# Optimization experiments

Hardware: AMD Instinct MI355X
Metric: run time of the kernel (lower is better)

Reference implementation:

```python
import jax, jax.numpy as jnp
import numpy as np

B, S, D, H, L, I, V, T = 8, 512, 768, 12, 6, 3072, 30522, 2
DH = D // H  # 64


def ln2d(x, g, b, eps=1e-5):
    # LayerNorm over the last two dims ([S, D]), affine params shaped [S, D]
    mu = jnp.mean(x, axis=(-2, -1), keepdims=True)
    var = jnp.var(x, axis=(-2, -1), keepdims=True)
    return (x - mu) * jax.lax.rsqrt(var + eps) * g + b


def setup_inputs() -> dict:
    key = jax.random.key(0)
    ks = jax.random.split(key, 16)
    s = 0.02
    inp = {
        "input_ids": jax.random.randint(ks[0], (B, S), 0, V, dtype=jnp.int32),
        "segment_ids": jax.random.randint(ks[1], (B, S), 0, T, dtype=jnp.int32),
        "input_mask": jnp.ones((B, S), dtype=jnp.float32),
        "word_emb": jax.random.normal(ks[2], (V, D), jnp.float32) * s,
        "seg_emb": jax.random.normal(ks[3], (T, D), jnp.float32) * s,
        "pos_emb": jax.random.normal(ks[4], (S, D), jnp.float32) * s,
        "ln0_g": jnp.ones((S, D), jnp.float32),
        "ln0_b": jnp.zeros((S, D), jnp.float32),
        "Wq": jax.random.normal(ks[5], (L, D, D), jnp.float32) * s,
        "Wk": jax.random.normal(ks[6], (L, D, D), jnp.float32) * s,
        "Wv": jax.random.normal(ks[7], (L, D, D), jnp.float32) * s,
        "W1": jax.random.normal(ks[8], (L, D, D), jnp.float32) * s,
        "b1": jnp.zeros((L, D), jnp.float32),
        "Wi": jax.random.normal(ks[9], (L, D, I), jnp.float32) * s,
        "bi": jnp.zeros((L, I), jnp.float32),
        "W2": jax.random.normal(ks[10], (L, I, D), jnp.float32) * s,
        "b2": jnp.zeros((L, D), jnp.float32),
        "lng": jnp.ones((L, S, D), jnp.float32),
        "lnb": jnp.zeros((L, S, D), jnp.float32),
        "Wp": jax.random.normal(ks[11], (D, 2), jnp.float32) * s,
        "bp": jnp.zeros((2,), jnp.float32),
    }
    return inp


def _forward(input_ids, segment_ids, input_mask, word_emb, seg_emb, pos_emb,
             ln0_g, ln0_b, Wq, Wk, Wv, W1, b1, Wi, bi, W2, b2, lng, lnb, Wp, bp):
    # embedding (word + segment + position), then 2-D LayerNorm
    x = word_emb[input_ids] + seg_emb[segment_ids] + pos_emb  # [B,S,D]
    x = ln2d(x, ln0_g, ln0_b)
    # multiplicative attention mask, broadcast over heads and KEY axis
    qmask = input_mask[:, None, :, None]  # [B,1,S,1]
    scale = 1.0 / jnp.sqrt(jnp.asarray(DH, x.dtype))
    for l in range(L):
        prev = x
        q = (x @ Wq[l]).reshape(B, S, H, DH).transpose(0, 2, 1, 3)
        k = (x @ Wk[l]).reshape(B, S, H, DH).transpose(0, 2, 1, 3)
        v = (x @ Wv[l]).reshape(B, S, H, DH).transpose(0, 2, 1, 3)
        scores = jnp.einsum('bhqd,bhkd->bhqk', q, k) * scale
        scores = scores * qmask  # multiplicative mask (as in source)
        probs = jax.nn.softmax(scores, axis=-1)
        attn = jnp.einsum('bhqk,bhkd->bhqd', probs, v)
        attn = attn.transpose(0, 2, 1, 3).reshape(B, S, D)
        h = jax.nn.relu(attn @ W1[l] + b1[l])
        h = jax.nn.relu(h @ Wi[l] + bi[l])
        h = jax.nn.relu(h @ W2[l] + b2[l])
        x = ln2d(h + prev, lng[l], lnb[l])
    logits = x @ Wp + bp  # [B,S,2]
    logits = logits + (1.0 - input_mask)[:, :, None] * (-1e4)
    return logits[:, :, 0], logits[:, :, 1]


def reference(input_ids, segment_ids, input_mask, word_emb, seg_emb, pos_emb,
              ln0_g, ln0_b, Wq, Wk, Wv, W1, b1, Wi, bi, W2, b2, lng, lnb, Wp, bp):
    return _forward(input_ids, segment_ids, input_mask, word_emb, seg_emb, pos_emb,
                    ln0_g, ln0_b, Wq, Wk, Wv, W1, b1, Wi, bi, W2, b2, lng, lnb, Wp, bp)
```

## Files before the change

### kernel.cpp

```cpp
#include <hip/hip_runtime.h>
#include <cstdint>
#include <cstddef>

typedef __bf16 bf16x8 __attribute__((ext_vector_type(8)));
typedef float f32x4 __attribute__((ext_vector_type(4)));
typedef unsigned short u16;

#define NB 8
#define NS 512
#define ND 768
#define NH 12
#define NL 6
#define NI 3072
#define NROWS (NB*NS)
#define SD (NS*ND)
#define MN ((size_t)NROWS*ND)

__device__ __forceinline__ u16 f2bf(float f) {
  union { float f; unsigned u; } v; v.f = f;
  unsigned r = v.u + 0x7fffu + ((v.u >> 16) & 1u);
  return (u16)(r >> 16);
}
__device__ __forceinline__ float b2f(u16 u) {
  union { unsigned u; float f; } v; v.u = ((unsigned)u) << 16; return v.f;
}

#define GLL(gsrc, ldst) \
  __builtin_amdgcn_global_load_lds((__attribute__((address_space(1))) void*)(gsrc), \
                                   (__attribute__((address_space(3))) void*)(ldst), 16, 0, 0)

#define CHS 4168

__global__ __launch_bounds__(256) void wconv_k(
    const float* __restrict__ Wq, const float* __restrict__ Wk, const float* __restrict__ Wv,
    const float* __restrict__ W1, const float* __restrict__ Wi, const float* __restrict__ W2,
    u16* __restrict__ wqkv_t, u16* __restrict__ w1_t, u16* __restrict__ wi_t, u16* __restrict__ w2_t)
{
  int bid = blockIdx.x;
  int l = bid / 864, r = bid % 864;
  const float* src; u16* dst; int Csrc, dstLD, tr, tc;
  if (r < 216) {
    int which = r / 72, t2 = r % 72;
    src = (which == 0 ? Wq : (which == 1 ? Wk : Wv)) + (size_t)l * ND * ND;
    dst = wqkv_t + (size_t)l * 2304 * ND + (size_t)which * ND * ND;
    Csrc = ND; dstLD = ND; tr = t2 / 12; tc = t2 % 12;
  } else if (r < 288) {
    int t2 = r - 216;
    src = W1 + (size_t)l * ND * ND; dst = w1_t + (size_t)l * ND * ND;
    Csrc = ND; dstLD = ND; tr = t2 / 12; tc = t2 % 12;
  } else if (r < 576) {
    int t2 = r - 288;
    src = Wi + (size_t)l * ND * NI; dst = wi_t + (size_t)l * ND * NI;
    Csrc = NI; dstLD = ND; tr = t2 / 48; tc = t2 % 48;
  } else {
    int t2 = r - 576;
    src = W2 + (size_t)l * ND * NI; dst = w2_t + (size_t)l * ND * NI;
    Csrc = ND; dstLD = NI; tr = t2 / 12; tc = t2 % 12;
  }
  __shared__ u16 lds[2 * CHS];
  int t0 = threadIdx.x;
  {
    int rrow = t0 >> 3, c0 = (t0 & 7) * 8;
    float4 va[4], vb[4];
    #pragma unroll
    for (int q = 0; q < 4; q++) {
      const float* sp = src + (size_t)(tr * 128 + q * 32 + rrow) * Csrc + tc * 64 + c0;
      va[q] = *reinterpret_cast<const float4*>(sp);
      vb[q] = *reinterpret_cast<const float4*>(sp + 4);
    }
    #pragma unroll
    for (int q = 0; q < 4; q++) {
      int row = q * 32 + rrow;
      u16* lp = &lds[(row >> 6) * CHS + (row & 63) * 65 + c0];
      lp[0] = f2bf(va[q].x); lp[1] = f2bf(va[q].y); lp[2] = f2bf(va[q].z); lp[3] = f2bf(va[q].w);
      lp[4] = f2bf(vb[q].x); lp[5] = f2bf(vb[q].y); lp[6] = f2bf(vb[q].z); lp[7] = f2bf(vb[q].w);
    }
  }
  __syncthreads();
  {
    int qq = t0 & 15;
    int rb = t0 >> 4;
    int ch = qq >> 3;
    int r6b = (qq & 7) * 8;
    #pragma unroll
    for (int p = 0; p < 4; p++) {
      int dstrow = p * 16 + rb;
      const u16* lq = &lds[ch * CHS + dstrow];
      unsigned res[4];
      #pragma unroll
      for (int e = 0; e < 4; e++) {
        unsigned lo = lq[(r6b + 2 * e) * 65];
        unsigned hi = lq[(r6b + 2 * e + 1) * 65];
        res[e] = lo | (hi << 16);
      }
      u16* dp = dst + (size_t)(tc * 64 + dstrow) * dstLD + tr * 128 + qq * 8;
      *reinterpret_cast<uint4*>(dp) = make_uint4(res[0], res[1], res[2], res[3]);
    }
  }
}

__global__ __launch_bounds__(256) void embed_ln_k(const int* __restrict__ ids,
    const int* __restrict__ segs, const float* __restrict__ wemb,
    const float* __restrict__ semb, const float* __restrict__ pemb,
    float* __restrict__ out, float* __restrict__ part)
{
  int b = blockIdx.x >> 6, c = blockIdx.x & 63;
  int base_row = b * NS + c * 8;
  int t = threadIdx.x;
  float s = 0.f, sq = 0.f;
  #pragma unroll
  for (int j = 0; j < 6; j++) {
    int fi = t + j * 256;
    int riw = fi / 192, col4 = fi - riw * 192;
    int row = base_row + riw;
    int id = ids[row], sg = segs[row];
    int srow = row & (NS - 1);
    float4 a = reinterpret_cast<const float4*>(wemb + (size_t)id * ND)[col4];
    float4 bb = reinterpret_cast<const float4*>(semb + (size_t)sg * ND)[col4];
    float4 cc = reinterpret_cast<const float4*>(pemb + (size_t)srow * ND)[col4];
    float y0 = a.x + bb.x + cc.x, y1 = a.y + bb.y + cc.y;
    float y2 = a.z + bb.z + cc.z, y3 = a.w + bb.w + cc.w;
    float4 o; o.x = y0; o.y = y1; o.z = y2; o.w = y3;
    reinterpret_cast<float4*>(out)[(size_t)row * 192 + col4] = o;
    s += y0 + y1 + y2 + y3;
    sq += y0 * y0 + y1 * y1 + y2 * y2 + y3 * y3;
  }
  #pragma unroll
  for (int d = 1; d < 64; d <<= 1) { s += __shfl_xor(s, d); sq += __shfl_xor(sq, d); }
  __shared__ float red[8];
  int w = t >> 6, lane = t & 63;
  if (lane == 0) { red[w] = s; red[4 + w] = sq; }
  __syncthreads();
  if (t == 0) {
    part[blockIdx.x * 2 + 0] = red[0] + red[1] + red[2] + red[3];
    part[blockIdx.x * 2 + 1] = red[4] + red[5] + red[6] + red[7];
  }
}

__global__ __launch_bounds__(256) void ln_apply_k(const float* __restrict__ x,
    const float* __restrict__ g, const float* __restrict__ bta, const float* __restrict__ part,
    u16* __restrict__ xb)
{
  int idx = blockIdx.x * 256 + threadIdx.x;
  int e = idx * 4;
  int b = e / SD;
  int sd = e - b * SD;
  int lane = threadIdx.x & 63;
  float s = part[b * 128 + lane * 2 + 0];
  float q = part[b * 128 + lane * 2 + 1];
  #pragma unroll
  for (int d = 1; d < 64; d <<= 1) { s += __shfl_xor(s, d); q += __shfl_xor(q, d); }
  float inv = 1.f / (float)SD;
  float mu = s * inv;
  float rstd = rsqrtf(q * inv - mu * mu + 1e-5f);
  float4 v = reinterpret_cast<const float4*>(x)[idx];
  float4 gg = reinterpret_cast<const float4*>(g)[sd >> 2];
  float4 bb = reinterpret_cast<const float4*>(bta)[sd >> 2];
  float y0 = (v.x - mu) * rstd * gg.x + bb.x;
  float y1 = (v.y - mu) * rstd * gg.y + bb.y;
  float y2 = (v.z - mu) * rstd * gg.z + bb.z;
  float y3 = (v.w - mu) * rstd * gg.w + bb.w;
  reinterpret_cast<ushort4*>(xb)[idx] = make_ushort4(f2bf(y0), f2bf(y1), f2bf(y2), f2bf(y3));
}

__global__ __launch_bounds__(256) void finw1_k(const u16* __restrict__ P,
    const float* __restrict__ bias, u16* __restrict__ out)
{
  size_t idx = (size_t)blockIdx.x * 256 + threadIdx.x;
  ushort4 p0 = reinterpret_cast<const ushort4*>(P)[idx];
  ushort4 p1 = reinterpret_cast<const ushort4*>(P)[idx + (MN >> 2)];
  ushort4 p2 = reinterpret_cast<const ushort4*>(P)[idx + 2 * (MN >> 2)];
  ushort4 p3 = reinterpret_cast<const ushort4*>(P)[idx + 3 * (MN >> 2)];
  int col4 = (int)((idx * 4) % ND) >> 2;
  float4 bv = reinterpret_cast<const float4*>(bias)[col4];
  float y0 = fmaxf(b2f(p0.x) + b2f(p1.x) + b2f(p2.x) + b2f(p3.x) + bv.x, 0.f);
  float y1 = fmaxf(b2f(p0.y) + b2f(p1.y) + b2f(p2.y) + b2f(p3.y) + bv.y, 0.f);
  float y2 = fmaxf(b2f(p0.z) + b2f(p1.z) + b2f(p2.z) + b2f(p3.z) + bv.z, 0.f);
  float y3 = fmaxf(b2f(p0.w) + b2f(p1.w) + b2f(p2.w) + b2f(p3.w) + bv.w, 0.f);
  reinterpret_cast<ushort4*>(out)[idx] = make_ushort4(f2bf(y0), f2bf(y1), f2bf(y2), f2bf(y3));
}

__global__ __launch_bounds__(256) void finw2_k(const u16* __restrict__ P,
    const float* __restrict__ bias, const u16* __restrict__ resid,
    float* __restrict__ ln_in, float* __restrict__ part)
{
  int b = blockIdx.x >> 6, c = blockIdx.x & 63;
  size_t f4base = ((size_t)b * SD + (size_t)c * 6144) >> 2;
  int t = threadIdx.x;
  float s = 0.f, sq = 0.f;
  #pragma unroll
  for (int j = 0; j < 6; j++) {
    size_t fi = f4base + t + j * 256;
    ushort4 p0 = reinterpret_cast<const ushort4*>(P)[fi];
    ushort4 p1 = reinterpret_cast<const ushort4*>(P)[fi + (MN >> 2)];
    ushort4 p2 = reinterpret_cast<const ushort4*>(P)[fi + 2 * (MN >> 2)];
    ushort4 p3 = reinterpret_cast<const ushort4*>(P)[fi + 3 * (MN >> 2)];
    ushort4 rv = reinterpret_cast<const ushort4*>(resid)[fi];
    int col4 = (((t + j * 256) * 4) % ND) >> 2;
    float4 bv = reinterpret_cast<const float4*>(bias)[col4];
    float y0 = fmaxf(b2f(p0.x) + b2f(p1.x) + b2f(p2.x) + b2f(p3.x) + bv.x, 0.f) + b2f(rv.x);
    float y1 = fmaxf(b2f(p0.y) + b2f(p1.y) + b2f(p2.y) + b2f(p3.y) + bv.y, 0.f) + b2f(rv.y);
    float y2 = fmaxf(b2f(p0.z) + b2f(p1.z) + b2f(p2.z) + b2f(p3.z) + bv.z, 0.f) + b2f(rv.z);
    float y3 = fmaxf(b2f(p0.w) + b2f(p1.w) + b2f(p2.w) + b2f(p3.w) + bv.w, 0.f) + b2f(rv.w);
    float4 o; o.x = y0; o.y = y1; o.z = y2; o.w = y3;
    reinterpret_cast<float4*>(ln_in)[fi] = o;
    s += y0 + y1 + y2 + y3;
    sq += y0 * y0 + y1 * y1 + y2 * y2 + y3 * y3;
  }
  #pragma unroll
  for (int d = 1; d < 64; d <<= 1) { s += __shfl_xor(s, d); sq += __shfl_xor(sq, d); }
  __shared__ float red[8];
  int w = t >> 6, lane = t & 63;
  if (lane == 0) { red[w] = s; red[4 + w] = sq; }
  __syncthreads();
  if (t == 0) {
    part[blockIdx.x * 2 + 0] = red[0] + red[1] + red[2] + red[3];
    part[blockIdx.x * 2 + 1] = red[4] + red[5] + red[6] + red[7];
  }
}

#define BM 128
#define BN 128
#define BK 32

template<int EPI>
__global__ __launch_bounds__(256) void gemm_bt(
    const u16* __restrict__ A, const u16* __restrict__ Bt, void* __restrict__ Cv,
    const float* __restrict__ bias, int M, int N, int K)
{
  __shared__ __align__(16) u16 As[2][BM * BK];
  __shared__ __align__(16) u16 Bs[2][BN * BK];
  const int gx = gridDim.x, gy = gridDim.y;
  int wg = (blockIdx.z * gy + blockIdx.y) * gx + blockIdx.x;
  int nwg = gx * gy * gridDim.z;
  int L = (wg & 7) * (nwg >> 3) + (wg >> 3);
  const int bx = L % gx, by = (L / gx) % gy, bz = L / (gx * gy);

  const int t = threadIdx.x;
  const int lane = t & 63, w = t >> 6;
  const int wr = w >> 1, wc = w & 1;
  const int l15 = lane & 15, lh = lane >> 4;
  const int m0 = by * BM, n0 = bx * BN;
  const int Ksub = K / gridDim.z;
  const int Koff = bz * Ksub;

  f32x4 acc[4][4];
  const f32x4 z4 = {0.f, 0.f, 0.f, 0.f};
  #pragma unroll
  for (int i = 0; i < 4; i++)
    #pragma unroll
    for (int j = 0; j < 4; j++) acc[i][j] = z4;

  const int ca = t, cb = t + 256;
  const u16* a0p = A + (size_t)(m0 + (ca >> 2)) * K + (ca & 3) * 8 + Koff;
  const u16* a1p = A + (size_t)(m0 + (cb >> 2)) * K + (cb & 3) * 8 + Koff;
  const u16* b0p = Bt + (size_t)(n0 + (ca >> 2)) * K + (ca & 3) * 8 + Koff;
  const u16* b1p = Bt + (size_t)(n0 + (cb >> 2)) * K + (cb & 3) * 8 + Koff;

  auto stage = [&](int buf, int k0) {
    GLL(a0p + k0, &As[buf][ca * 8]);
    GLL(a1p + k0, &As[buf][cb * 8]);
    GLL(b0p + k0, &Bs[buf][ca * 8]);
    GLL(b1p + k0, &Bs[buf][cb * 8]);
  };

  const int nt = Ksub / BK;
  stage(0, 0);
  __syncthreads();
  for (int it = 0; it < nt; ++it) {
    const int cur = it & 1;
    if (it + 1 < nt) stage(cur ^ 1, (it + 1) * BK);
    bf16x8 af[4], bfr[4];
    #pragma unroll
    for (int i = 0; i < 4; i++)
      af[i] = *reinterpret_cast<const bf16x8*>(&As[cur][(wr * 64 + i * 16 + l15) * BK + lh * 8]);
    #pragma unroll
    for (int j = 0; j < 4; j++)
      bfr[j] = *reinterpret_cast<const bf16x8*>(&Bs[cur][(wc * 64 + j * 16 + l15) * BK + lh * 8]);
    #pragma unroll
    for (int i = 0; i < 4; i++)
      #pragma unroll
      for (int j = 0; j < 4; j++)
        acc[i][j] = __builtin_amdgcn_mfma_f32_16x16x32_bf16(af[i], bfr[j], acc[i][j], 0, 0, 0);
    __syncthreads();
  }

  u16* PoutB = (u16*)Cv + (size_t)bz * M * N;
  #pragma unroll
  for (int i = 0; i < 4; i++) {
    int row_b = m0 + wr * 64 + i * 16 + lh * 4;
    #pragma unroll
    for (int j = 0; j < 4; j++) {
      int col = n0 + wc * 64 + j * 16 + l15;
      float bv = (EPI == 1) ? bias[col] : 0.f;
      #pragma unroll
      for (int r = 0; r < 4; r++) {
        size_t off = (size_t)(row_b + r) * N + col;
        float v = acc[i][j][r];
        if (EPI == 1) ((u16*)Cv)[off] = f2bf(fmaxf(v + bv, 0.f));
        else if (EPI == 3) PoutB[off] = f2bf(v);
        else ((u16*)Cv)[off] = f2bf(v);
      }
    }
  }
}

__global__ __launch_bounds__(256) void attn_k(
    const u16* __restrict__ qkv, const float* __restrict__ mask, u16* __restrict__ out)
{
  int wg = (blockIdx.z * 12 + blockIdx.y) * 8 + blockIdx.x;
  int L = (wg & 7) * 96 + (wg >> 3);
  const int qt = L & 7;
  const int h = (L >> 3) % 12;
  const int b = L / 96;
  __shared__ __align__(16) u16 Qs[64 * 64];
  __shared__ __align__(16) u16 Ks[64 * 72];
  __shared__ __align__(16) u16 Vt[64 * 72];
  __shared__ __align__(16) u16 Pw[4][16 * 72];
  const int t = threadIdx.x, lane = t & 63, w = t >> 6;
  const int l15 = lane & 15, lh = lane >> 4;

  #pragma unroll
  for (int p = 0; p < 2; p++) {
    int c = t + p * 256;
    const u16* src = qkv + (size_t)(b * NS + qt * 64 + (c >> 3)) * 2304 + h * 64 + (c & 7) * 8;
    GLL(src, Qs + c * 8);
  }
  __syncthreads();

  bf16x8 aq[2];
  #pragma unroll
  for (int kk = 0; kk < 2; kk++)
    aq[kk] = *reinterpret_cast<const bf16x8*>(&Qs[(w * 16 + l15) * 64 + kk * 32 + lh * 8]);

  float qm[4];
  #pragma unroll
  for (int r = 0; r < 4; r++)
    qm[r] = mask[b * NS + qt * 64 + w * 16 + lh * 4 + r] * 0.125f;

  float mrun[4], lrun[4];
  f32x4 o[4];
  const f32x4 z4 = {0.f, 0.f, 0.f, 0.f};
  #pragma unroll
  for (int r = 0; r < 4; r++) { mrun[r] = -3e38f; lrun[r] = 0.f; }
  #pragma unroll
  for (int jn = 0; jn < 4; jn++) o[jn] = z4;

  for (int kc = 0; kc < 8; kc++) {
    __syncthreads();
    #pragma unroll
    for (int p = 0; p < 2; p++) {
      int k = (t >> 3) + p * 32;
      int dh0 = (t & 7) * 8;
      const u16* ks = qkv + (size_t)(b * NS + kc * 64 + k) * 2304 + ND + h * 64 + dh0;
      uint4 kv4 = *reinterpret_cast<const uint4*>(ks);
      *reinterpret_cast<uint4*>(&Ks[k * 72 + dh0]) = kv4;
    }
    #pragma unroll
    for (int p = 0; p < 2; p++) {
      int k = (t >> 3) + p * 32;
      int dh0 = (t & 7) * 8;
      const u16* vs = qkv + (size_t)(b * NS + kc * 64 + k) * 2304 + 2 * ND + h * 64 + dh0;
      uint4 vv = *reinterpret_cast<const uint4*>(vs);
      Vt[(dh0 + 0) * 72 + k] = (u16)(vv.x & 0xffff);
      Vt[(dh0 + 1) * 72 + k] = (u16)(vv.x >> 16);
      Vt[(dh0 + 2) * 72 + k] = (u16)(vv.y & 0xffff);
      Vt[(dh0 + 3) * 72 + k] = (u16)(vv.y >> 16);
      Vt[(dh0 + 4) * 72 + k] = (u16)(vv.z & 0xffff);
      Vt[(dh0 + 5) * 72 + k] = (u16)(vv.z >> 16);
      Vt[(dh0 + 6) * 72 + k] = (u16)(vv.w & 0xffff);
      Vt[(dh0 + 7) * 72 + k] = (u16)(vv.w >> 16);
    }
    __syncthreads();

    f32x4 s[4];
    #pragma unroll
    for (int j = 0; j < 4; j++) s[j] = z4;
    #pragma unroll
    for (int kk = 0; kk < 2; kk++) {
      bf16x8 bk[4];
      #pragma unroll
      for (int j = 0; j < 4; j++)
        bk[j] = *reinterpret_cast<const bf16x8*>(&Ks[(j * 16 + l15) * 72 + kk * 32 + lh * 8]);
      #pragma unroll
      for (int j = 0; j < 4; j++)
        s[j] = __builtin_amdgcn_mfma_f32_16x16x32_bf16(aq[kk], bk[j], s[j], 0, 0, 0);
    }

    #pragma unroll
    for (int r = 0; r < 4; r++) {
      float q4 = qm[r];
      float v0 = s[0][r] * q4, v1 = s[1][r] * q4, v2 = s[2][r] * q4, v3 = s[3][r] * q4;
      float pm = fmaxf(fmaxf(v0, v1), fmaxf(v2, v3));
      pm = fmaxf(pm, __shfl_xor(pm, 1));
      pm = fmaxf(pm, __shfl_xor(pm, 2));
      pm = fmaxf(pm, __shfl_xor(pm, 4));
      pm = fmaxf(pm, __shfl_xor(pm, 8));
      float mnew = fmaxf(mrun[r], pm);
      float corr = __expf(mrun[r] - mnew);
      mrun[r] = mnew;
      float p0 = __expf(v0 - mnew), p1 = __expf(v1 - mnew);
      float p2 = __expf(v2 - mnew), p3 = __expf(v3 - mnew);
      s[0][r] = p0; s[1][r] = p1; s[2][r] = p2; s[3][r] = p3;
      float rs = p0 + p1 + p2 + p3;
      rs += __shfl_xor(rs, 1);
      rs += __shfl_xor(rs, 2);
      rs += __shfl_xor(rs, 4);
      rs += __shfl_xor(rs, 8);
      lrun[r] = lrun[r] * corr + rs;
      #pragma unroll
      for (int jn = 0; jn < 4; jn++) o[jn][r] *= corr;
    }
    #pragma unroll
    for (int j = 0; j < 4; j++)
      #pragma unroll
      for (int r = 0; r < 4; r++)
        Pw[w][(lh * 4 + r) * 72 + j * 16 + l15] = f2bf(s[j][r]);

    #pragma unroll
    for (int kk2 = 0; kk2 < 2; kk2++) {
      bf16x8 pa, vb[4];
      pa = *reinterpret_cast<const bf16x8*>(&Pw[w][l15 * 72 + kk2 * 32 + lh * 8]);
      #pragma unroll
      for (int jn = 0; jn < 4; jn++)
        vb[jn] = *reinterpret_cast<const bf16x8*>(&Vt[(jn * 16 + l15) * 72 + kk2 * 32 + lh * 8]);
      #pragma unroll
      for (int jn = 0; jn < 4; jn++)
        o[jn] = __builtin_amdgcn_mfma_f32_16x16x32_bf16(pa, vb[jn], o[jn], 0, 0, 0);
    }
  }

  #pragma unroll
  for (int r = 0; r < 4; r++) {
    int q = qt * 64 + w * 16 + lh * 4 + r;
    float invl = 1.f / lrun[r];
    #pragma unroll
    for (int jn = 0; jn < 4; jn++) {
      int col = h * 64 + jn * 16 + l15;
      out[(size_t)(b * NS + q) * ND + col] = f2bf(o[jn][r] * invl);
    }
  }
}

__global__ __launch_bounds__(256) void logits_k(const u16* __restrict__ x,
    const float* __restrict__ Wp, const float* __restrict__ bp, const float* __restrict__ mask,
    float* __restrict__ out)
{
  int t = threadIdx.x, lane = t & 63, w = t >> 6;
  int row = blockIdx.x * 4 + w;
  const u16* xr = x + (size_t)row * ND;
  float a0 = 0.f, a1 = 0.f;
  for (int i = lane; i < ND; i += 64) {
    float v = b2f(xr[i]);
    a0 += v * Wp[i * 2 + 0];
    a1 += v * Wp[i * 2 + 1];
  }
  #pragma unroll
  for (int d = 1; d < 64; d <<= 1) { a0 += __shfl_xor(a0, d); a1 += __shfl_xor(a1, d); }
  if (lane == 0) {
    float pen = (1.f - mask[row]) * -10000.f;
    out[row] = a0 + bp[0] + pen;
    out[NROWS + row] = a1 + bp[1] + pen;
  }
}

extern "C" void kernel_launch(void* const* d_in, const int* in_sizes, int n_in,
                              void* d_out, int out_size, void* d_ws, size_t ws_size,
                              hipStream_t stream)
{
  const int* ids = (const int*)d_in[0];
  const int* segs = (const int*)d_in[1];
  const float* mask = (const float*)d_in[2];
  const float* wemb = (const float*)d_in[3];
  const float* semb = (const float*)d_in[4];
  const float* pemb = (const float*)d_in[5];
  const float* ln0g = (const float*)d_in[6];
  const float* ln0b = (const float*)d_in[7];
  const float* Wq = (const float*)d_in[8];
  const float* Wk = (const float*)d_in[9];
  const float* Wv = (const float*)d_in[10];
  const float* W1 = (const float*)d_in[11];
  const float* b1 = (const float*)d_in[12];
  const float* Wi = (const float*)d_in[13];
  const float* bi = (const float*)d_in[14];
  const float* W2 = (const float*)d_in[15];
  const float* b2 = (const float*)d_in[16];
  const float* lng = (const float*)d_in[17];
  const float* lnb = (const float*)d_in[18];
  const float* Wp = (const float*)d_in[19];
  const float* bp = (const float*)d_in[20];

  char* ws = (char*)d_ws;
  size_t o = 0;
  auto alloc = [&](size_t n) { size_t r = o; o += (n + 255) & ~(size_t)255; return r; };
  u16* wqkv_t = (u16*)(ws + alloc((size_t)NL * 2304 * ND * 2));
  u16* w1_t   = (u16*)(ws + alloc((size_t)NL * ND * ND * 2));
  u16* wi_t   = (u16*)(ws + alloc((size_t)NL * ND * NI * 2));
  u16* w2_t   = (u16*)(ws + alloc((size_t)NL * ND * NI * 2));
  u16* x_bf16  = (u16*)(ws + alloc((size_t)NROWS * ND * 2));
  u16* qkv     = (u16*)(ws + alloc((size_t)NROWS * 2304 * 2));
  u16* attn    = (u16*)(ws + alloc((size_t)NROWS * ND * 2));
  u16* h1      = (u16*)(ws + alloc((size_t)NROWS * ND * 2));
  u16* hi      = (u16*)(ws + alloc((size_t)NROWS * NI * 2));
  float* ln_in = (float*)(ws + alloc((size_t)NROWS * ND * 4));
  u16* pbuf    = (u16*)(ws + alloc(4 * MN * 2));
  float* part  = (float*)(ws + alloc(512 * 2 * 4));

  wconv_k<<<NL * 864, 256, 0, stream>>>(Wq, Wk, Wv, W1, Wi, W2, wqkv_t, w1_t, wi_t, w2_t);
  embed_ln_k<<<512, 256, 0, stream>>>(ids, segs, wemb, semb, pemb, ln_in, part);
  ln_apply_k<<<3072, 256, 0, stream>>>(ln_in, ln0g, ln0b, part, x_bf16);

  for (int l = 0; l < NL; l++) {
    gemm_bt<0><<<dim3(18, 32), 256, 0, stream>>>(x_bf16, wqkv_t + (size_t)l * 2304 * ND, qkv,
                                                 nullptr, NROWS, 2304, ND);
    attn_k<<<dim3(8, NH, NB), 256, 0, stream>>>(qkv, mask, attn);
    gemm_bt<3><<<dim3(6, 32, 4), 256, 0, stream>>>(attn, w1_t + (size_t)l * ND * ND, pbuf,
                                                   nullptr, NROWS, ND, ND);
    finw1_k<<<3072, 256, 0, stream>>>(pbuf, b1 + (size_t)l * ND, h1);
    gemm_bt<1><<<dim3(24, 32), 256, 0, stream>>>(h1, wi_t + (size_t)l * ND * NI, hi,
                                                 bi + (size_t)l * NI, NROWS, NI, ND);
    gemm_bt<3><<<dim3(6, 32, 4), 256, 0, stream>>>(hi, w2_t + (size_t)l * ND * NI, pbuf,
                                                   nullptr, NROWS, ND, NI);
    finw2_k<<<512, 256, 0, stream>>>(pbuf, b2 + (size_t)l * ND, x_bf16, ln_in, part);
    ln_apply_k<<<3072, 256, 0, stream>>>(ln_in, lng + (size_t)l * SD, lnb + (size_t)l * SD, part, x_bf16);
  }

  logits_k<<<1024, 256, 0, stream>>>(x_bf16, Wp, bp, mask, (float*)d_out);
}
```

Before: 976.3 us.

## Store LN intermediates in bf16 and emit transposed V from QKV GEMM epilogue

The pre-LayerNorm buffer written by the embedding and residual kernels changes from fp32 to bf16, halving its write and read traffic. Statistics are still accumulated in fp32 before rounding. The QKV GEMM gets a new epilogue that also scatters V into a per-head transposed layout, so attention can load V tiles with vector copies instead of scalar LDS transposes. This costs extra strided 2-byte global stores in the GEMM epilogue and slightly lowers LayerNorm input precision.

```diff
diff --git a/kernel.cpp b/kernel.cpp
--- a/kernel.cpp
+++ b/kernel.cpp
@@ -102,7 +102,7 @@
 __global__ __launch_bounds__(256) void embed_ln_k(const int* __restrict__ ids,
     const int* __restrict__ segs, const float* __restrict__ wemb,
     const float* __restrict__ semb, const float* __restrict__ pemb,
-    float* __restrict__ out, float* __restrict__ part)
+    u16* __restrict__ out, float* __restrict__ part)
 {
   int b = blockIdx.x >> 6, c = blockIdx.x & 63;
   int base_row = b * NS + c * 8;
@@ -120,8 +120,8 @@
     float4 cc = reinterpret_cast<const float4*>(pemb + (size_t)srow * ND)[col4];
     float y0 = a.x + bb.x + cc.x, y1 = a.y + bb.y + cc.y;
     float y2 = a.z + bb.z + cc.z, y3 = a.w + bb.w + cc.w;
-    float4 o; o.x = y0; o.y = y1; o.z = y2; o.w = y3;
-    reinterpret_cast<float4*>(out)[(size_t)row * 192 + col4] = o;
+    reinterpret_cast<ushort4*>(out)[(size_t)row * 192 + col4] =
+        make_ushort4(f2bf(y0), f2bf(y1), f2bf(y2), f2bf(y3));
     s += y0 + y1 + y2 + y3;
     sq += y0 * y0 + y1 * y1 + y2 * y2 + y3 * y3;
   }
@@ -137,7 +137,7 @@
   }
 }
 
-__global__ __launch_bounds__(256) void ln_apply_k(const float* __restrict__ x,
+__global__ __launch_bounds__(256) void ln_apply_k(const u16* __restrict__ x,
     const float* __restrict__ g, const float* __restrict__ bta, const float* __restrict__ part,
     u16* __restrict__ xb)
 {
@@ -153,13 +153,13 @@
   float inv = 1.f / (float)SD;
   float mu = s * inv;
   float rstd = rsqrtf(q * inv - mu * mu + 1e-5f);
-  float4 v = reinterpret_cast<const float4*>(x)[idx];
+  ushort4 v = reinterpret_cast<const ushort4*>(x)[idx];
   float4 gg = reinterpret_cast<const float4*>(g)[sd >> 2];
   float4 bb = reinterpret_cast<const float4*>(bta)[sd >> 2];
-  float y0 = (v.x - mu) * rstd * gg.x + bb.x;
-  float y1 = (v.y - mu) * rstd * gg.y + bb.y;
-  float y2 = (v.z - mu) * rstd * gg.z + bb.z;
-  float y3 = (v.w - mu) * rstd * gg.w + bb.w;
+  float y0 = (b2f(v.x) - mu) * rstd * gg.x + bb.x;
+  float y1 = (b2f(v.y) - mu) * rstd * gg.y + bb.y;
+  float y2 = (b2f(v.z) - mu) * rstd * gg.z + bb.z;
+  float y3 = (b2f(v.w) - mu) * rstd * gg.w + bb.w;
   reinterpret_cast<ushort4*>(xb)[idx] = make_ushort4(f2bf(y0), f2bf(y1), f2bf(y2), f2bf(y3));
 }
 
@@ -182,7 +182,7 @@
 
 __global__ __launch_bounds__(256) void finw2_k(const u16* __restrict__ P,
     const float* __restrict__ bias, const u16* __restrict__ resid,
-    float* __restrict__ ln_in, float* __restrict__ part)
+    u16* __restrict__ ln_in, float* __restrict__ part)
 {
   int b = blockIdx.x >> 6, c = blockIdx.x & 63;
   size_t f4base = ((size_t)b * SD + (size_t)c * 6144) >> 2;
@@ -202,8 +202,7 @@
     float y1 = fmaxf(b2f(p0.y) + b2f(p1.y) + b2f(p2.y) + b2f(p3.y) + bv.y, 0.f) + b2f(rv.y);
     float y2 = fmaxf(b2f(p0.z) + b2f(p1.z) + b2f(p2.z) + b2f(p3.z) + bv.z, 0.f) + b2f(rv.z);
     float y3 = fmaxf(b2f(p0.w) + b2f(p1.w) + b2f(p2.w) + b2f(p3.w) + bv.w, 0.f) + b2f(rv.w);
-    float4 o; o.x = y0; o.y = y1; o.z = y2; o.w = y3;
-    reinterpret_cast<float4*>(ln_in)[fi] = o;
+    reinterpret_cast<ushort4*>(ln_in)[fi] = make_ushort4(f2bf(y0), f2bf(y1), f2bf(y2), f2bf(y3));
     s += y0 + y1 + y2 + y3;
     sq += y0 * y0 + y1 * y1 + y2 * y2 + y3 * y3;
   }
@@ -226,7 +225,7 @@
 template<int EPI>
 __global__ __launch_bounds__(256) void gemm_bt(
     const u16* __restrict__ A, const u16* __restrict__ Bt, void* __restrict__ Cv,
-    const float* __restrict__ bias, int M, int N, int K)
+    const float* __restrict__ bias, u16* __restrict__ vtr, int M, int N, int K)
 {
   __shared__ __align__(16) u16 As[2][BM * BK];
   __shared__ __align__(16) u16 Bs[2][BN * BK];
@@ -297,16 +296,26 @@
       for (int r = 0; r < 4; r++) {
         size_t off = (size_t)(row_b + r) * N + col;
         float v = acc[i][j][r];
+        u16 bf = f2bf(v);
         if (EPI == 1) ((u16*)Cv)[off] = f2bf(fmaxf(v + bv, 0.f));
-        else if (EPI == 3) PoutB[off] = f2bf(v);
-        else ((u16*)Cv)[off] = f2bf(v);
+        else if (EPI == 3) PoutB[off] = bf;
+        else {
+          ((u16*)Cv)[off] = bf;
+          if (EPI == 4 && col >= 1536) {
+            int vc = col - 1536;
+            int row = row_b + r;
+            int bb = row >> 9, ss = row & (NS - 1);
+            vtr[(((size_t)(bb * NH + (vc >> 6)) << 6) + (vc & 63)) * NS + ss] = bf;
+          }
+        }
       }
     }
   }
 }
 
 __global__ __launch_bounds__(256) void attn_k(
-    const u16* __restrict__ qkv, const float* __restrict__ mask, u16* __restrict__ out)
+    const u16* __restrict__ qkv, const u16* __restrict__ vtr,
+    const float* __restrict__ mask, u16* __restrict__ out)
 {
   int wg = (blockIdx.z * 12 + blockIdx.y) * 8 + blockIdx.x;
   int L = (wg & 7) * 96 + (wg >> 3);
@@ -346,6 +355,8 @@
   #pragma unroll
   for (int jn = 0; jn < 4; jn++) o[jn] = z4;
 
+  const u16* vbase = vtr + ((size_t)(b * NH + h) << 6) * NS;
+
   for (int kc = 0; kc < 8; kc++) {
     __syncthreads();
     #pragma unroll
@@ -358,18 +369,10 @@
     }
     #pragma unroll
     for (int p = 0; p < 2; p++) {
-      int k = (t >> 3) + p * 32;
-      int dh0 = (t & 7) * 8;
-      const u16* vs = qkv + (size_t)(b * NS + kc * 64 + k) * 2304 + 2 * ND + h * 64 + dh0;
-      uint4 vv = *reinterpret_cast<const uint4*>(vs);
-      Vt[(dh0 + 0) * 72 + k] = (u16)(vv.x & 0xffff);
-      Vt[(dh0 + 1) * 72 + k] = (u16)(vv.x >> 16);
-      Vt[(dh0 + 2) * 72 + k] = (u16)(vv.y & 0xffff);
-      Vt[(dh0 + 3) * 72 + k] = (u16)(vv.y >> 16);
-      Vt[(dh0 + 4) * 72 + k] = (u16)(vv.z & 0xffff);
-      Vt[(dh0 + 5) * 72 + k] = (u16)(vv.z >> 16);
-      Vt[(dh0 + 6) * 72 + k] = (u16)(vv.w & 0xffff);
-      Vt[(dh0 + 7) * 72 + k] = (u16)(vv.w >> 16);
+      int dh = (t >> 3) + p * 32;
+      int k8 = (t & 7) * 8;
+      uint4 vv = *reinterpret_cast<const uint4*>(vbase + (size_t)dh * NS + kc * 64 + k8);
+      *reinterpret_cast<uint4*>(&Vt[dh * 72 + k8]) = vv;
     }
     __syncthreads();
 
@@ -499,10 +502,11 @@
   u16* w2_t   = (u16*)(ws + alloc((size_t)NL * ND * NI * 2));
   u16* x_bf16  = (u16*)(ws + alloc((size_t)NROWS * ND * 2));
   u16* qkv     = (u16*)(ws + alloc((size_t)NROWS * 2304 * 2));
+  u16* vtr     = (u16*)(ws + alloc((size_t)NROWS * ND * 2));
   u16* attn    = (u16*)(ws + alloc((size_t)NROWS * ND * 2));
   u16* h1      = (u16*)(ws + alloc((size_t)NROWS * ND * 2));
   u16* hi      = (u16*)(ws + alloc((size_t)NROWS * NI * 2));
-  float* ln_in = (float*)(ws + alloc((size_t)NROWS * ND * 4));
+  u16* ln_in   = (u16*)(ws + alloc((size_t)NROWS * ND * 2));
   u16* pbuf    = (u16*)(ws + alloc(4 * MN * 2));
   float* part  = (float*)(ws + alloc(512 * 2 * 4));
 
@@ -511,16 +515,16 @@
   ln_apply_k<<<3072, 256, 0, stream>>>(ln_in, ln0g, ln0b, part, x_bf16);
 
   for (int l = 0; l < NL; l++) {
-    gemm_bt<0><<<dim3(18, 32), 256, 0, stream>>>(x_bf16, wqkv_t + (size_t)l * 2304 * ND, qkv,
-                                                 nullptr, NROWS, 2304, ND);
-    attn_k<<<dim3(8, NH, NB), 256, 0, stream>>>(qkv, mask, attn);
+    gemm_bt<4><<<dim3(18, 32), 256, 0, stream>>>(x_bf16, wqkv_t + (size_t)l * 2304 * ND, qkv,
+                                                 nullptr, vtr, NROWS, 2304, ND);
+    attn_k<<<dim3(8, NH, NB), 256, 0, stream>>>(qkv, vtr, mask, attn);
     gemm_bt<3><<<dim3(6, 32, 4), 256, 0, stream>>>(attn, w1_t + (size_t)l * ND * ND, pbuf,
-                                                   nullptr, NROWS, ND, ND);
+                                                   nullptr, nullptr, NROWS, ND, ND);
     finw1_k<<<3072, 256, 0, stream>>>(pbuf, b1 + (size_t)l * ND, h1);
     gemm_bt<1><<<dim3(24, 32), 256, 0, stream>>>(h1, wi_t + (size_t)l * ND * NI, hi,
-                                                 bi + (size_t)l * NI, NROWS, NI, ND);
+                                                 bi + (size_t)l * NI, nullptr, NROWS, NI, ND);
     gemm_bt<3><<<dim3(6, 32, 4), 256, 0, stream>>>(hi, w2_t + (size_t)l * ND * NI, pbuf,
-                                                   nullptr, NROWS, ND, NI);
+                                                   nullptr, nullptr, NROWS, ND, NI);
     finw2_k<<<512, 256, 0, stream>>>(pbuf, b2 + (size_t)l * ND, x_bf16, ln_in, part);
     ln_apply_k<<<3072, 256, 0, stream>>>(ln_in, lng + (size_t)l * SD, lnb + (size_t)l * SD, part, x_bf16);
   }
```

Result: slower. 1.012 ms (+3.6%).
